# Performance work log

Hardware: AMD Instinct MI355X
Metric: run time of the kernel (lower is better)

The kernel has to match this reference:

```python
import jax, jax.numpy as jnp
import numpy as np

EMB = 1024
HEADS = 16
HEAD_DIM = EMB // HEADS
N = 16384


def setup_inputs() -> dict:
    key = jax.random.key(0)
    ks = jax.random.split(key, 9)
    s = 1.0 / np.sqrt(EMB)
    return {
        "src": jax.random.normal(ks[0], (N, EMB), dtype=jnp.float32),
        "Wq": jax.random.normal(ks[1], (EMB, EMB), dtype=jnp.float32) * s,
        "bq": jax.random.normal(ks[2], (EMB,), dtype=jnp.float32) * s,
        "Wk": jax.random.normal(ks[3], (EMB, EMB), dtype=jnp.float32) * s,
        "bk": jax.random.normal(ks[4], (EMB,), dtype=jnp.float32) * s,
        "Wv": jax.random.normal(ks[5], (EMB, EMB), dtype=jnp.float32) * s,
        "bv": jax.random.normal(ks[6], (EMB,), dtype=jnp.float32) * s,
        "Wo": jax.random.normal(ks[7], (EMB, EMB), dtype=jnp.float32) * s,
        "bo": jax.random.normal(ks[8], (EMB,), dtype=jnp.float32) * s,
    }


def reference(src, Wq, bq, Wk, bk, Wv, bv, Wo, bo):
    # nn.Linear: y = x @ W^T + b  (W is [out, in])
    q = src @ Wq.T + bq          # [N, E]
    k = src @ Wk.T + bk
    v = src @ Wv.T + bv
    q = q.reshape(-1, HEADS, HEAD_DIM)   # [N, H, D]
    k = k.reshape(-1, HEADS, HEAD_DIM)
    v = v.reshape(-1, HEADS, HEAD_DIM)
    # NOTE: attention is across heads within each token: scores [N, H, H]
    scale = 1.0 / jnp.sqrt(jnp.float32(HEAD_DIM))
    scores = jnp.einsum('nhd,ngd->nhg', q, k) * scale   # [N, H, H]
    attn = jax.nn.softmax(scores, axis=-1)
    out = jnp.einsum('nhg,ngd->nhd', attn, v)            # [N, H, D]
    out = out.reshape(-1, EMB)
    out = out @ Wo.T + bo                                 # [N, E]
    return out.reshape(-1, HEADS, HEAD_DIM)               # [N, H, D]
```

## Files before the change

kernel.cpp:

```cpp
#include <hip/hip_runtime.h>
#include <stdint.h>
#include <stddef.h>

#define EMB 1024
#define NTOK 16384

typedef __attribute__((ext_vector_type(8))) short short8;
typedef __attribute__((ext_vector_type(4))) float floatx4;

__device__ __forceinline__ unsigned short f2bf(float f) {
    union { float f; unsigned int u; } v; v.f = f;
    unsigned int u = v.u;
    unsigned int r = (u + 0x7fffu + ((u >> 16) & 1u)) >> 16;
    return (unsigned short)r;
}
__device__ __forceinline__ float bf2f(unsigned short s) {
    union { unsigned int u; float f; } v; v.u = ((unsigned int)s) << 16;
    return v.f;
}

__device__ __forceinline__ void gload16(const void* g, void* l) {
    __builtin_amdgcn_global_load_lds(
        (const __attribute__((address_space(1))) void*)g,
        (__attribute__((address_space(3))) void*)l, 16, 0, 0);
}

__global__ void cvt_kernel(const float* __restrict__ in,
                           unsigned short* __restrict__ out, int n4) {
    int idx = blockIdx.x * blockDim.x + threadIdx.x;
    int stride = gridDim.x * blockDim.x;
    for (int i = idx; i < n4; i += stride) {
        float4 f = reinterpret_cast<const float4*>(in)[i];
        ushort4 o;
        o.x = f2bf(f.x); o.y = f2bf(f.y); o.z = f2bf(f.z); o.w = f2bf(f.w);
        reinterpret_cast<ushort4*>(out)[i] = o;
    }
}

__global__ void cvt4_kernel(const float* __restrict__ s0, const float* __restrict__ s1,
                            const float* __restrict__ s2, const float* __restrict__ s3,
                            unsigned short* __restrict__ out) {
    int idx = blockIdx.x * blockDim.x + threadIdx.x;
    const int total = 4 << 18;
    int stride = gridDim.x * blockDim.x;
    for (int i = idx; i < total; i += stride) {
        int w = i >> 18, r = i & ((1 << 18) - 1);
        const float* s = (w == 0) ? s0 : (w == 1) ? s1 : (w == 2) ? s2 : s3;
        float4 f = reinterpret_cast<const float4*>(s)[r];
        ushort4 o;
        o.x = f2bf(f.x); o.y = f2bf(f.y); o.z = f2bf(f.z); o.w = f2bf(f.w);
        reinterpret_cast<ushort4*>(out)[i] = o;
    }
}

__global__ void bias_cat_kernel(const float* __restrict__ b0,
                                const float* __restrict__ b1,
                                const float* __restrict__ b2,
                                float* __restrict__ out) {
    int i = blockIdx.x * blockDim.x + threadIdx.x;
    float v = (i < 1024) ? b0[i] : (i < 2048 ? b1[i - 1024] : b2[i - 2048]);
    out[i] = v;
}

__device__ __forceinline__ void store_val(float* C, size_t idx, float v) { C[idx] = v; }
__device__ __forceinline__ void store_val(unsigned short* C, size_t idx, float v) { C[idx] = f2bf(v); }

template<typename OUT_T>
__global__ __launch_bounds__(512, 2)
void gemm256(const unsigned short* __restrict__ A,
             const unsigned short* __restrict__ B,
             const float* __restrict__ bias,
             OUT_T* __restrict__ C,
             int K, int Nc, int grid_m)
{
    __shared__ unsigned short lds[65536];

    const int bid = blockIdx.x;
    const int x = bid & 7;
    const int w = bid >> 3;
    const int ms = grid_m >> 3;
    const int m0 = (x * ms + (w & (ms - 1))) * 256;
    const int n0 = (w / ms) * 256;

    const int tid  = threadIdx.x;
    const int lane = tid & 63;
    const int wid  = tid >> 6;
    const int wm = (wid >> 2) * 128;
    const int wn = (wid & 3) * 64;
    const int rr = lane & 15;
    const int klo = (((lane >> 4) ^ ((rr >> 1) & 3)) << 3);

    const int aro = (wm + rr) * 32 + klo;
    const int bro = 16384 + (wn + rr) * 32 + klo;

    const unsigned short* pA[2];
    const unsigned short* pB[2];
    int ldst[2];
#pragma unroll
    for (int l = 0; l < 2; ++l) {
        const int P16  = l * 512 + tid;
        const int rowS = P16 >> 2;
        const int colel = (((P16 & 3) ^ ((rowS >> 1) & 3)) << 3);
        pA[l] = A + (size_t)(m0 + rowS) * K + colel;
        pB[l] = B + (size_t)(n0 + rowS) * K + colel;
        ldst[l] = P16 * 8;
    }

    floatx4 acc[8][4];
#pragma unroll
    for (int i = 0; i < 8; ++i)
#pragma unroll
        for (int j = 0; j < 4; ++j)
            acc[i][j] = (floatx4){0.f, 0.f, 0.f, 0.f};

    const int NT = K >> 6;

#pragma unroll
    for (int l = 0; l < 2; ++l) {
        gload16(pA[l],      &lds[0     + ldst[l]]);
        gload16(pA[l] + 32, &lds[8192  + ldst[l]]);
        gload16(pB[l],      &lds[16384 + ldst[l]]);
        gload16(pB[l] + 32, &lds[24576 + ldst[l]]);
    }
    asm volatile("s_waitcnt vmcnt(0)" ::: "memory");
    asm volatile("s_barrier" ::: "memory");

    short8 a0[4], a1[4], b0[4];
#pragma unroll
    for (int i = 0; i < 4; ++i)
        a0[i] = *reinterpret_cast<const short8*>(&lds[aro + i * 512]);
#pragma unroll
    for (int j = 0; j < 4; ++j)
        b0[j] = *reinterpret_cast<const short8*>(&lds[bro + j * 512]);

    for (int t = 0; t < NT; ++t) {
        const int cur = (t & 1) * 32768;
        const int nxt = cur ^ 32768;
        const int ktn = (t + 1 < NT) ? (t + 1) * 64 : 0;

        gload16(pA[0] + ktn, &lds[nxt + ldst[0]]);
        gload16(pA[1] + ktn, &lds[nxt + ldst[1]]);
        gload16(pB[0] + ktn, &lds[nxt + 16384 + ldst[0]]);
        gload16(pB[1] + ktn, &lds[nxt + 16384 + ldst[1]]);
#pragma unroll
        for (int i = 0; i < 4; ++i)
            a1[i] = *reinterpret_cast<const short8*>(&lds[cur + aro + 2048 + i * 512]);
        __builtin_amdgcn_s_setprio(1);
#pragma unroll
        for (int j = 0; j < 4; ++j)
#pragma unroll
            for (int i = 0; i < 4; ++i)
                acc[i][j] = __builtin_amdgcn_mfma_f32_16x16x32_bf16(a0[i], b0[j], acc[i][j], 0, 0, 0);
#pragma unroll
        for (int j = 0; j < 4; ++j)
#pragma unroll
            for (int i = 0; i < 4; ++i)
                acc[4 + i][j] = __builtin_amdgcn_mfma_f32_16x16x32_bf16(a1[i], b0[j], acc[4 + i][j], 0, 0, 0);
        __builtin_amdgcn_s_setprio(0);
        asm volatile("s_waitcnt vmcnt(4)" ::: "memory");
        asm volatile("s_barrier" ::: "memory");

        gload16(pA[0] + ktn + 32, &lds[nxt + 8192 + ldst[0]]);
        gload16(pA[1] + ktn + 32, &lds[nxt + 8192 + ldst[1]]);
        gload16(pB[0] + ktn + 32, &lds[nxt + 24576 + ldst[0]]);
        gload16(pB[1] + ktn + 32, &lds[nxt + 24576 + ldst[1]]);
#pragma unroll
        for (int i = 0; i < 4; ++i)
            a0[i] = *reinterpret_cast<const short8*>(&lds[cur + 8192 + aro + i * 512]);
#pragma unroll
        for (int j = 0; j < 4; ++j)
            b0[j] = *reinterpret_cast<const short8*>(&lds[cur + 8192 + bro + j * 512]);
#pragma unroll
        for (int i = 0; i < 4; ++i)
            a1[i] = *reinterpret_cast<const short8*>(&lds[cur + 8192 + aro + 2048 + i * 512]);
        __builtin_amdgcn_s_setprio(1);
#pragma unroll
        for (int j = 0; j < 4; ++j)
#pragma unroll
            for (int i = 0; i < 4; ++i)
                acc[i][j] = __builtin_amdgcn_mfma_f32_16x16x32_bf16(a0[i], b0[j], acc[i][j], 0, 0, 0);
#pragma unroll
        for (int j = 0; j < 4; ++j)
#pragma unroll
            for (int i = 0; i < 4; ++i)
                acc[4 + i][j] = __builtin_amdgcn_mfma_f32_16x16x32_bf16(a1[i], b0[j], acc[4 + i][j], 0, 0, 0);
        __builtin_amdgcn_s_setprio(0);
        asm volatile("s_waitcnt vmcnt(4)" ::: "memory");
        asm volatile("s_barrier" ::: "memory");
#pragma unroll
        for (int i = 0; i < 4; ++i)
            a0[i] = *reinterpret_cast<const short8*>(&lds[nxt + aro + i * 512]);
#pragma unroll
        for (int j = 0; j < 4; ++j)
            b0[j] = *reinterpret_cast<const short8*>(&lds[nxt + bro + j * 512]);
    }

    const int cn  = lane & 15;
    const int cm4 = (lane >> 4) * 4;
    float bv[4];
#pragma unroll
    for (int j = 0; j < 4; ++j) bv[j] = bias[n0 + wn + j * 16 + cn];
#pragma unroll
    for (int ai = 0; ai < 8; ++ai) {
        const int row = m0 + wm + (ai >> 2) * 64 + (ai & 3) * 16 + cm4;
#pragma unroll
        for (int j = 0; j < 4; ++j) {
            const int col = n0 + wn + j * 16 + cn;
#pragma unroll
            for (int r = 0; r < 4; ++r)
                store_val(C, (size_t)(row + r) * Nc + col, acc[ai][j][r] + bv[j]);
        }
    }
}

#define ROWP 72

__global__ __launch_bounds__(256)
void attn_kernel(const unsigned short* __restrict__ QKV,
                 unsigned short* __restrict__ O)
{
    const int wave = threadIdx.x >> 6;
    const int lane = threadIdx.x & 63;
    const int n = blockIdx.x * 4 + wave;

    __shared__ unsigned short lq[4][16 * ROWP];
    __shared__ unsigned short lk[4][16 * ROWP];
    __shared__ unsigned short lv[4][16 * ROWP];
    __shared__ float lp[4][256];

    {
        const unsigned short* gq = QKV + (size_t)n * 3072;
        const unsigned short* gk = gq + 1024;
        const unsigned short* gv = gq + 2048;
        for (int t = lane; t < 128; t += 64) {
            int r = t >> 3, c = t & 7;
            *reinterpret_cast<short8*>(&lq[wave][r * ROWP + c * 8]) =
                *reinterpret_cast<const short8*>(gq + t * 8);
            *reinterpret_cast<short8*>(&lk[wave][r * ROWP + c * 8]) =
                *reinterpret_cast<const short8*>(gk + t * 8);
            *reinterpret_cast<short8*>(&lv[wave][r * ROWP + c * 8]) =
                *reinterpret_cast<const short8*>(gv + t * 8);
        }
    }
    __syncthreads();

    const int g = lane & 15;
    const int a = lane >> 4;

    float kf[64];
#pragma unroll
    for (int c2 = 0; c2 < 8; ++c2) {
        short8 kv = *reinterpret_cast<const short8*>(&lk[wave][g * ROWP + c2 * 8]);
#pragma unroll
        for (int e = 0; e < 8; ++e) kf[c2 * 8 + e] = bf2f((unsigned short)kv[e]);
    }

#pragma unroll
    for (int i = 0; i < 4; ++i) {
        const int h = i * 4 + a;
        float s = 0.f;
#pragma unroll
        for (int c2 = 0; c2 < 8; ++c2) {
            short8 qv = *reinterpret_cast<const short8*>(&lq[wave][h * ROWP + c2 * 8]);
#pragma unroll
            for (int e = 0; e < 8; ++e)
                s = fmaf(bf2f((unsigned short)qv[e]), kf[c2 * 8 + e], s);
        }
        s *= 0.125f;

        float m = s;
#pragma unroll
        for (int o = 1; o < 16; o <<= 1) m = fmaxf(m, __shfl_xor(m, o, 64));
        float p = expf(s - m);
        float sum = p;
#pragma unroll
        for (int o = 1; o < 16; o <<= 1) sum += __shfl_xor(sum, o, 64);
        lp[wave][h * 16 + g] = p / sum;
    }
    __syncthreads();

    const int h = lane >> 2;
    const int db = (lane & 3) * 16;
    float o[16];
#pragma unroll
    for (int e = 0; e < 16; ++e) o[e] = 0.f;

    for (int g2 = 0; g2 < 16; ++g2) {
        const float pw = lp[wave][h * 16 + g2];
        short8 v0 = *reinterpret_cast<const short8*>(&lv[wave][g2 * ROWP + db]);
        short8 v1 = *reinterpret_cast<const short8*>(&lv[wave][g2 * ROWP + db + 8]);
#pragma unroll
        for (int e = 0; e < 8; ++e) {
            o[e]     = fmaf(pw, bf2f((unsigned short)v0[e]), o[e]);
            o[8 + e] = fmaf(pw, bf2f((unsigned short)v1[e]), o[8 + e]);
        }
    }

    short8 o0, o1;
#pragma unroll
    for (int e = 0; e < 8; ++e) {
        o0[e] = (short)f2bf(o[e]);
        o1[e] = (short)f2bf(o[8 + e]);
    }
    unsigned short* dst = O + (size_t)n * EMB + h * 64 + db;
    *reinterpret_cast<short8*>(dst) = o0;
    *reinterpret_cast<short8*>(dst + 8) = o1;
}

extern "C" void kernel_launch(void* const* d_in, const int* in_sizes, int n_in,
                              void* d_out, int out_size, void* d_ws, size_t ws_size,
                              hipStream_t stream)
{
    const float* src = (const float*)d_in[0];
    const float* Wq  = (const float*)d_in[1];
    const float* bq  = (const float*)d_in[2];
    const float* Wk  = (const float*)d_in[3];
    const float* bk  = (const float*)d_in[4];
    const float* Wv  = (const float*)d_in[5];
    const float* bv  = (const float*)d_in[6];
    const float* Wo  = (const float*)d_in[7];
    const float* bo  = (const float*)d_in[8];
    float* out = (float*)d_out;

    unsigned short* ws = (unsigned short*)d_ws;
    unsigned short* src_bf = ws;
    unsigned short* wqkv   = src_bf + (size_t)NTOK * EMB;
    unsigned short* wo_bf  = wqkv + (size_t)3 * EMB * EMB;
    unsigned short* qkv    = wo_bf + (size_t)EMB * EMB;
    unsigned short* ab     = qkv + (size_t)NTOK * 3 * EMB;
    float* bias_cat        = (float*)(ab + (size_t)NTOK * EMB);

    cvt_kernel<<<2048, 256, 0, stream>>>(src, src_bf, NTOK * EMB / 4);
    cvt4_kernel<<<2048, 256, 0, stream>>>(Wq, Wk, Wv, Wo, wqkv);
    bias_cat_kernel<<<12, 256, 0, stream>>>(bq, bk, bv, bias_cat);

    gemm256<unsigned short><<<dim3(64 * 12), 512, 0, stream>>>(
        src_bf, wqkv, bias_cat, qkv, EMB, 3 * EMB, 64);

    attn_kernel<<<NTOK / 4, 256, 0, stream>>>(qkv, ab);

    gemm256<float><<<dim3(64 * 4), 512, 0, stream>>>(
        ab, wo_bf, bo, out, EMB, EMB, 64);
}
```

Baseline: 200.2 us.

## Make GEMM persistent over N tiles with one 256-block wave

The GEMM kernel now launches exactly 256 workgroups, and each one loops over several 256-wide N tiles for its M tile. The K-tile prefetch carries straight across N-tile boundaries, and the epilogue with bias is emitted inside the loop. This removes the tail effect of 768 blocks on 256 CUs and keeps the A tile warm in cache. In exchange, occupancy drops to 1 block per CU (launch bounds changed from 2 to 1), and the epilogue stores are no longer overlapped by other resident blocks.

```diff
diff --git a/kernel.cpp b/kernel.cpp
--- a/kernel.cpp
+++ b/kernel.cpp
@@ -66,21 +66,22 @@
 __device__ __forceinline__ void store_val(unsigned short* C, size_t idx, float v) { C[idx] = f2bf(v); }
 
 template<typename OUT_T>
-__global__ __launch_bounds__(512, 2)
-void gemm256(const unsigned short* __restrict__ A,
-             const unsigned short* __restrict__ B,
-             const float* __restrict__ bias,
-             OUT_T* __restrict__ C,
-             int K, int Nc, int grid_m)
+__global__ __launch_bounds__(512, 1)
+void gemm256mn(const unsigned short* __restrict__ A,
+               const unsigned short* __restrict__ B,
+               const float* __restrict__ bias,
+               OUT_T* __restrict__ C,
+               int Nc, int nt_n)
 {
     __shared__ unsigned short lds[65536];
+    const int K = 1024;
+    const int NT = 16;
 
     const int bid = blockIdx.x;
     const int x = bid & 7;
     const int w = bid >> 3;
-    const int ms = grid_m >> 3;
-    const int m0 = (x * ms + (w & (ms - 1))) * 256;
-    const int n0 = (w / ms) * 256;
+    const int m0 = (x * 8 + (w & 7)) * 256;
+    const int n_base = (w >> 3) * nt_n * 256;
 
     const int tid  = threadIdx.x;
     const int lane = tid & 63;
@@ -102,9 +103,10 @@
         const int rowS = P16 >> 2;
         const int colel = (((P16 & 3) ^ ((rowS >> 1) & 3)) << 3);
         pA[l] = A + (size_t)(m0 + rowS) * K + colel;
-        pB[l] = B + (size_t)(n0 + rowS) * K + colel;
+        pB[l] = B + (size_t)(n_base + rowS) * K + colel;
         ldst[l] = P16 * 8;
     }
+    const size_t nstep = (size_t)256 * K;
 
     floatx4 acc[8][4];
 #pragma unroll
@@ -113,7 +115,7 @@
         for (int j = 0; j < 4; ++j)
             acc[i][j] = (floatx4){0.f, 0.f, 0.f, 0.f};
 
-    const int NT = K >> 6;
+    const int TOT = nt_n * NT;
 
 #pragma unroll
     for (int l = 0; l < 2; ++l) {
@@ -133,15 +135,22 @@
     for (int j = 0; j < 4; ++j)
         b0[j] = *reinterpret_cast<const short8*>(&lds[bro + j * 512]);
 
-    for (int t = 0; t < NT; ++t) {
-        const int cur = (t & 1) * 32768;
+    const int cn  = lane & 15;
+    const int cm4 = (lane >> 4) * 4;
+
+    for (int vt = 0; vt < TOT; ++vt) {
+        const int cur = (vt & 1) * 32768;
         const int nxt = cur ^ 32768;
-        const int ktn = (t + 1 < NT) ? (t + 1) * 64 : 0;
+        int vtn = vt + 1; if (vtn == TOT) vtn = 0;
+        const int ktn = (vtn & 15) * 64;
+        const int nbn = vtn >> 4;
+        const unsigned short* pBn0 = pB[0] + (size_t)nbn * nstep + ktn;
+        const unsigned short* pBn1 = pB[1] + (size_t)nbn * nstep + ktn;
 
         gload16(pA[0] + ktn, &lds[nxt + ldst[0]]);
         gload16(pA[1] + ktn, &lds[nxt + ldst[1]]);
-        gload16(pB[0] + ktn, &lds[nxt + 16384 + ldst[0]]);
-        gload16(pB[1] + ktn, &lds[nxt + 16384 + ldst[1]]);
+        gload16(pBn0,        &lds[nxt + 16384 + ldst[0]]);
+        gload16(pBn1,        &lds[nxt + 16384 + ldst[1]]);
 #pragma unroll
         for (int i = 0; i < 4; ++i)
             a1[i] = *reinterpret_cast<const short8*>(&lds[cur + aro + 2048 + i * 512]);
@@ -162,8 +171,8 @@
 
         gload16(pA[0] + ktn + 32, &lds[nxt + 8192 + ldst[0]]);
         gload16(pA[1] + ktn + 32, &lds[nxt + 8192 + ldst[1]]);
-        gload16(pB[0] + ktn + 32, &lds[nxt + 24576 + ldst[0]]);
-        gload16(pB[1] + ktn + 32, &lds[nxt + 24576 + ldst[1]]);
+        gload16(pBn0 + 32,        &lds[nxt + 24576 + ldst[0]]);
+        gload16(pBn1 + 32,        &lds[nxt + 24576 + ldst[1]]);
 #pragma unroll
         for (int i = 0; i < 4; ++i)
             a0[i] = *reinterpret_cast<const short8*>(&lds[cur + 8192 + aro + i * 512]);
@@ -193,22 +202,28 @@
 #pragma unroll
         for (int j = 0; j < 4; ++j)
             b0[j] = *reinterpret_cast<const short8*>(&lds[nxt + bro + j * 512]);
-    }
-
-    const int cn  = lane & 15;
-    const int cm4 = (lane >> 4) * 4;
-    float bv[4];
-#pragma unroll
-    for (int j = 0; j < 4; ++j) bv[j] = bias[n0 + wn + j * 16 + cn];
-#pragma unroll
-    for (int ai = 0; ai < 8; ++ai) {
-        const int row = m0 + wm + (ai >> 2) * 64 + (ai & 3) * 16 + cm4;
-#pragma unroll
-        for (int j = 0; j < 4; ++j) {
-            const int col = n0 + wn + j * 16 + cn;
-#pragma unroll
-            for (int r = 0; r < 4; ++r)
-                store_val(C, (size_t)(row + r) * Nc + col, acc[ai][j][r] + bv[j]);
+
+        if ((vt & 15) == 15) {
+            const int n0 = n_base + (vt >> 4) * 256;
+            float bv[4];
+#pragma unroll
+            for (int j = 0; j < 4; ++j) bv[j] = bias[n0 + wn + j * 16 + cn];
+#pragma unroll
+            for (int ai = 0; ai < 8; ++ai) {
+                const int row = m0 + wm + (ai >> 2) * 64 + (ai & 3) * 16 + cm4;
+#pragma unroll
+                for (int j = 0; j < 4; ++j) {
+                    const int col = n0 + wn + j * 16 + cn;
+#pragma unroll
+                    for (int r = 0; r < 4; ++r)
+                        store_val(C, (size_t)(row + r) * Nc + col, acc[ai][j][r] + bv[j]);
+                }
+            }
+#pragma unroll
+            for (int i = 0; i < 8; ++i)
+#pragma unroll
+                for (int j = 0; j < 4; ++j)
+                    acc[i][j] = (floatx4){0.f, 0.f, 0.f, 0.f};
         }
     }
 }
@@ -334,11 +349,11 @@
     cvt4_kernel<<<2048, 256, 0, stream>>>(Wq, Wk, Wv, Wo, wqkv);
     bias_cat_kernel<<<12, 256, 0, stream>>>(bq, bk, bv, bias_cat);
 
-    gemm256<unsigned short><<<dim3(64 * 12), 512, 0, stream>>>(
-        src_bf, wqkv, bias_cat, qkv, EMB, 3 * EMB, 64);
+    gemm256mn<unsigned short><<<dim3(256), 512, 0, stream>>>(
+        src_bf, wqkv, bias_cat, qkv, 3 * EMB, 3);
 
     attn_kernel<<<NTOK / 4, 256, 0, stream>>>(qkv, ab);
 
-    gemm256<float><<<dim3(64 * 4), 512, 0, stream>>>(
-        ab, wo_bf, bo, out, EMB, EMB, 64);
-}
+    gemm256mn<float><<<dim3(256), 512, 0, stream>>>(
+        ab, wo_bf, bo, out, EMB, 1);
+}
```

Result: no change. 201.2 us (+0.5%).

## Switch GEMMs to 32x32x16 MFMA and fuse conversion kernels into one launch

Applied to the files above, without the earlier changes.

The GEMM inner loop now uses 32x32x16 bf16 MFMA instructions instead of 16x16x32, with 16-wide accumulators and LDS fragment reads re-mapped through an XOR on the k-group. The epilogue is rewritten to match the 32x32 output layout. This cuts instruction count and LDS fragment traffic per FLOP. The launch bound drops to one block per CU, which matches the 128KB LDS footprint. The src, weight and bias conversion kernels are merged into a single launch to remove launch overhead.

```diff
diff --git a/kernel.cpp b/kernel.cpp
--- a/kernel.cpp
+++ b/kernel.cpp
@@ -7,6 +7,7 @@
 
 typedef __attribute__((ext_vector_type(8))) short short8;
 typedef __attribute__((ext_vector_type(4))) float floatx4;
+typedef __attribute__((ext_vector_type(16))) float floatx16;
 
 __device__ __forceinline__ unsigned short f2bf(float f) {
     union { float f; unsigned int u; } v; v.f = f;
@@ -25,49 +26,51 @@
         (__attribute__((address_space(3))) void*)l, 16, 0, 0);
 }
 
-__global__ void cvt_kernel(const float* __restrict__ in,
-                           unsigned short* __restrict__ out, int n4) {
+__global__ void cvt_all(const float* __restrict__ src,
+                        const float* __restrict__ s0, const float* __restrict__ s1,
+                        const float* __restrict__ s2, const float* __restrict__ s3,
+                        const float* __restrict__ b0, const float* __restrict__ b1,
+                        const float* __restrict__ b2,
+                        unsigned short* __restrict__ src_bf,
+                        unsigned short* __restrict__ wout,
+                        float* __restrict__ bias_cat) {
+    if (blockIdx.x == 0) {
+#pragma unroll
+        for (int t = 0; t < 12; ++t) {
+            int i = t * 256 + threadIdx.x;
+            float v = (i < 1024) ? b0[i] : (i < 2048 ? b1[i - 1024] : b2[i - 2048]);
+            bias_cat[i] = v;
+        }
+    }
+    const int SRC4 = 1 << 22;
+    const int TOT4 = SRC4 + (1 << 20);
     int idx = blockIdx.x * blockDim.x + threadIdx.x;
     int stride = gridDim.x * blockDim.x;
-    for (int i = idx; i < n4; i += stride) {
-        float4 f = reinterpret_cast<const float4*>(in)[i];
+    for (int i = idx; i < TOT4; i += stride) {
+        const float* sp;
+        unsigned short* op;
+        int r;
+        if (i < SRC4) {
+            sp = src; op = src_bf; r = i;
+        } else {
+            int j = i - SRC4;
+            int w = j >> 18; r = j & ((1 << 18) - 1);
+            sp = (w == 0) ? s0 : (w == 1) ? s1 : (w == 2) ? s2 : s3;
+            op = wout + ((size_t)(i - SRC4) & ~((size_t)(1 << 18) - 1)) * 4;
+        }
+        float4 f = reinterpret_cast<const float4*>(sp)[r];
         ushort4 o;
         o.x = f2bf(f.x); o.y = f2bf(f.y); o.z = f2bf(f.z); o.w = f2bf(f.w);
-        reinterpret_cast<ushort4*>(out)[i] = o;
-    }
-}
-
-__global__ void cvt4_kernel(const float* __restrict__ s0, const float* __restrict__ s1,
-                            const float* __restrict__ s2, const float* __restrict__ s3,
-                            unsigned short* __restrict__ out) {
-    int idx = blockIdx.x * blockDim.x + threadIdx.x;
-    const int total = 4 << 18;
-    int stride = gridDim.x * blockDim.x;
-    for (int i = idx; i < total; i += stride) {
-        int w = i >> 18, r = i & ((1 << 18) - 1);
-        const float* s = (w == 0) ? s0 : (w == 1) ? s1 : (w == 2) ? s2 : s3;
-        float4 f = reinterpret_cast<const float4*>(s)[r];
-        ushort4 o;
-        o.x = f2bf(f.x); o.y = f2bf(f.y); o.z = f2bf(f.z); o.w = f2bf(f.w);
-        reinterpret_cast<ushort4*>(out)[i] = o;
-    }
-}
-
-__global__ void bias_cat_kernel(const float* __restrict__ b0,
-                                const float* __restrict__ b1,
-                                const float* __restrict__ b2,
-                                float* __restrict__ out) {
-    int i = blockIdx.x * blockDim.x + threadIdx.x;
-    float v = (i < 1024) ? b0[i] : (i < 2048 ? b1[i - 1024] : b2[i - 2048]);
-    out[i] = v;
+        reinterpret_cast<ushort4*>(op)[r] = o;
+    }
 }
 
 __device__ __forceinline__ void store_val(float* C, size_t idx, float v) { C[idx] = v; }
 __device__ __forceinline__ void store_val(unsigned short* C, size_t idx, float v) { C[idx] = f2bf(v); }
 
 template<typename OUT_T>
-__global__ __launch_bounds__(512, 2)
-void gemm256(const unsigned short* __restrict__ A,
+__global__ __launch_bounds__(512, 1)
+void gemm32s(const unsigned short* __restrict__ A,
              const unsigned short* __restrict__ B,
              const float* __restrict__ bias,
              OUT_T* __restrict__ C,
@@ -87,11 +90,12 @@
     const int wid  = tid >> 6;
     const int wm = (wid >> 2) * 128;
     const int wn = (wid & 3) * 64;
-    const int rr = lane & 15;
-    const int klo = (((lane >> 4) ^ ((rr >> 1) & 3)) << 3);
-
-    const int aro = (wm + rr) * 32 + klo;
-    const int bro = 16384 + (wn + rr) * 32 + klo;
+    const int rl = lane & 31;
+    const int lh = lane >> 5;
+    const int go = ((lh ^ ((rl >> 1) & 3)) << 3);
+
+    const int arB = (wm + rl) * 32 + go;
+    const int brB = 16384 + (wn + rl) * 32 + go;
 
     const unsigned short* pA[2];
     const unsigned short* pB[2];
@@ -106,12 +110,13 @@
         ldst[l] = P16 * 8;
     }
 
-    floatx4 acc[8][4];
-#pragma unroll
-    for (int i = 0; i < 8; ++i)
-#pragma unroll
-        for (int j = 0; j < 4; ++j)
-            acc[i][j] = (floatx4){0.f, 0.f, 0.f, 0.f};
+    floatx16 acc[4][2];
+#pragma unroll
+    for (int i = 0; i < 4; ++i)
+#pragma unroll
+        for (int j = 0; j < 2; ++j)
+            acc[i][j] = (floatx16){0.f,0.f,0.f,0.f,0.f,0.f,0.f,0.f,
+                                   0.f,0.f,0.f,0.f,0.f,0.f,0.f,0.f};
 
     const int NT = K >> 6;
 
@@ -125,13 +130,13 @@
     asm volatile("s_waitcnt vmcnt(0)" ::: "memory");
     asm volatile("s_barrier" ::: "memory");
 
-    short8 a0[4], a1[4], b0[4];
-#pragma unroll
-    for (int i = 0; i < 4; ++i)
-        a0[i] = *reinterpret_cast<const short8*>(&lds[aro + i * 512]);
-#pragma unroll
-    for (int j = 0; j < 4; ++j)
-        b0[j] = *reinterpret_cast<const short8*>(&lds[bro + j * 512]);
+    short8 a0[4], a1[4], b0[2], b1[2];
+#pragma unroll
+    for (int fm = 0; fm < 4; ++fm)
+        a0[fm] = *reinterpret_cast<const short8*>(&lds[arB + fm * 1024]);
+#pragma unroll
+    for (int fn = 0; fn < 2; ++fn)
+        b0[fn] = *reinterpret_cast<const short8*>(&lds[brB + fn * 1024]);
 
     for (int t = 0; t < NT; ++t) {
         const int cur = (t & 1) * 32768;
@@ -143,19 +148,22 @@
         gload16(pB[0] + ktn, &lds[nxt + 16384 + ldst[0]]);
         gload16(pB[1] + ktn, &lds[nxt + 16384 + ldst[1]]);
 #pragma unroll
-        for (int i = 0; i < 4; ++i)
-            a1[i] = *reinterpret_cast<const short8*>(&lds[cur + aro + 2048 + i * 512]);
+        for (int fm = 0; fm < 4; ++fm)
+            a1[fm] = *reinterpret_cast<const short8*>(&lds[cur + ((arB + fm * 1024) ^ 16)]);
+#pragma unroll
+        for (int fn = 0; fn < 2; ++fn)
+            b1[fn] = *reinterpret_cast<const short8*>(&lds[cur + ((brB + fn * 1024) ^ 16)]);
         __builtin_amdgcn_s_setprio(1);
 #pragma unroll
-        for (int j = 0; j < 4; ++j)
-#pragma unroll
-            for (int i = 0; i < 4; ++i)
-                acc[i][j] = __builtin_amdgcn_mfma_f32_16x16x32_bf16(a0[i], b0[j], acc[i][j], 0, 0, 0);
-#pragma unroll
-        for (int j = 0; j < 4; ++j)
-#pragma unroll
-            for (int i = 0; i < 4; ++i)
-                acc[4 + i][j] = __builtin_amdgcn_mfma_f32_16x16x32_bf16(a1[i], b0[j], acc[4 + i][j], 0, 0, 0);
+        for (int fn = 0; fn < 2; ++fn)
+#pragma unroll
+            for (int fm = 0; fm < 4; ++fm)
+                acc[fm][fn] = __builtin_amdgcn_mfma_f32_32x32x16_bf16(a0[fm], b0[fn], acc[fm][fn], 0, 0, 0);
+#pragma unroll
+        for (int fn = 0; fn < 2; ++fn)
+#pragma unroll
+            for (int fm = 0; fm < 4; ++fm)
+                acc[fm][fn] = __builtin_amdgcn_mfma_f32_32x32x16_bf16(a1[fm], b1[fn], acc[fm][fn], 0, 0, 0);
         __builtin_amdgcn_s_setprio(0);
         asm volatile("s_waitcnt vmcnt(4)" ::: "memory");
         asm volatile("s_barrier" ::: "memory");
@@ -165,50 +173,54 @@
         gload16(pB[0] + ktn + 32, &lds[nxt + 24576 + ldst[0]]);
         gload16(pB[1] + ktn + 32, &lds[nxt + 24576 + ldst[1]]);
 #pragma unroll
-        for (int i = 0; i < 4; ++i)
-            a0[i] = *reinterpret_cast<const short8*>(&lds[cur + 8192 + aro + i * 512]);
-#pragma unroll
-        for (int j = 0; j < 4; ++j)
-            b0[j] = *reinterpret_cast<const short8*>(&lds[cur + 8192 + bro + j * 512]);
-#pragma unroll
-        for (int i = 0; i < 4; ++i)
-            a1[i] = *reinterpret_cast<const short8*>(&lds[cur + 8192 + aro + 2048 + i * 512]);
+        for (int fm = 0; fm < 4; ++fm)
+            a0[fm] = *reinterpret_cast<const short8*>(&lds[cur + 8192 + arB + fm * 1024]);
+#pragma unroll
+        for (int fn = 0; fn < 2; ++fn)
+            b0[fn] = *reinterpret_cast<const short8*>(&lds[cur + 8192 + brB + fn * 1024]);
+#pragma unroll
+        for (int fm = 0; fm < 4; ++fm)
+            a1[fm] = *reinterpret_cast<const short8*>(&lds[cur + 8192 + ((arB + fm * 1024) ^ 16)]);
+#pragma unroll
+        for (int fn = 0; fn < 2; ++fn)
+            b1[fn] = *reinterpret_cast<const short8*>(&lds[cur + 8192 + ((brB + fn * 1024) ^ 16)]);
         __builtin_amdgcn_s_setprio(1);
 #pragma unroll
-        for (int j = 0; j < 4; ++j)
-#pragma unroll
-            for (int i = 0; i < 4; ++i)
-                acc[i][j] = __builtin_amdgcn_mfma_f32_16x16x32_bf16(a0[i], b0[j], acc[i][j], 0, 0, 0);
-#pragma unroll
-        for (int j = 0; j < 4; ++j)
-#pragma unroll
-            for (int i = 0; i < 4; ++i)
-                acc[4 + i][j] = __builtin_amdgcn_mfma_f32_16x16x32_bf16(a1[i], b0[j], acc[4 + i][j], 0, 0, 0);
+        for (int fn = 0; fn < 2; ++fn)
+#pragma unroll
+            for (int fm = 0; fm < 4; ++fm)
+                acc[fm][fn] = __builtin_amdgcn_mfma_f32_32x32x16_bf16(a0[fm], b0[fn], acc[fm][fn], 0, 0, 0);
+#pragma unroll
+        for (int fn = 0; fn < 2; ++fn)
+#pragma unroll
+            for (int fm = 0; fm < 4; ++fm)
+                acc[fm][fn] = __builtin_amdgcn_mfma_f32_32x32x16_bf16(a1[fm], b1[fn], acc[fm][fn], 0, 0, 0);
         __builtin_amdgcn_s_setprio(0);
         asm volatile("s_waitcnt vmcnt(4)" ::: "memory");
         asm volatile("s_barrier" ::: "memory");
 #pragma unroll
-        for (int i = 0; i < 4; ++i)
-            a0[i] = *reinterpret_cast<const short8*>(&lds[nxt + aro + i * 512]);
-#pragma unroll
-        for (int j = 0; j < 4; ++j)
-            b0[j] = *reinterpret_cast<const short8*>(&lds[nxt + bro + j * 512]);
-    }
-
-    const int cn  = lane & 15;
-    const int cm4 = (lane >> 4) * 4;
-    float bv[4];
-#pragma unroll
-    for (int j = 0; j < 4; ++j) bv[j] = bias[n0 + wn + j * 16 + cn];
-#pragma unroll
-    for (int ai = 0; ai < 8; ++ai) {
-        const int row = m0 + wm + (ai >> 2) * 64 + (ai & 3) * 16 + cm4;
-#pragma unroll
-        for (int j = 0; j < 4; ++j) {
-            const int col = n0 + wn + j * 16 + cn;
-#pragma unroll
-            for (int r = 0; r < 4; ++r)
-                store_val(C, (size_t)(row + r) * Nc + col, acc[ai][j][r] + bv[j]);
+        for (int fm = 0; fm < 4; ++fm)
+            a0[fm] = *reinterpret_cast<const short8*>(&lds[nxt + arB + fm * 1024]);
+#pragma unroll
+        for (int fn = 0; fn < 2; ++fn)
+            b0[fn] = *reinterpret_cast<const short8*>(&lds[nxt + brB + fn * 1024]);
+    }
+
+    const int col0 = n0 + wn + rl;
+    float bv[2];
+    bv[0] = bias[col0];
+    bv[1] = bias[col0 + 32];
+#pragma unroll
+    for (int fm = 0; fm < 4; ++fm) {
+        const int rbase = m0 + wm + fm * 32 + 4 * lh;
+#pragma unroll
+        for (int fn = 0; fn < 2; ++fn) {
+            const int col = col0 + fn * 32;
+#pragma unroll
+            for (int reg = 0; reg < 16; ++reg) {
+                const int row = rbase + (reg & 3) + 8 * (reg >> 2);
+                store_val(C, (size_t)row * Nc + col, acc[fm][fn][reg] + bv[fn]);
+            }
         }
     }
 }
@@ -330,15 +342,14 @@
     unsigned short* ab     = qkv + (size_t)NTOK * 3 * EMB;
     float* bias_cat        = (float*)(ab + (size_t)NTOK * EMB);
 
-    cvt_kernel<<<2048, 256, 0, stream>>>(src, src_bf, NTOK * EMB / 4);
-    cvt4_kernel<<<2048, 256, 0, stream>>>(Wq, Wk, Wv, Wo, wqkv);
-    bias_cat_kernel<<<12, 256, 0, stream>>>(bq, bk, bv, bias_cat);
-
-    gemm256<unsigned short><<<dim3(64 * 12), 512, 0, stream>>>(
+    cvt_all<<<2048, 256, 0, stream>>>(src, Wq, Wk, Wv, Wo, bq, bk, bv,
+                                      src_bf, wqkv, bias_cat);
+
+    gemm32s<unsigned short><<<dim3(64 * 12), 512, 0, stream>>>(
         src_bf, wqkv, bias_cat, qkv, EMB, 3 * EMB, 64);
 
     attn_kernel<<<NTOK / 4, 256, 0, stream>>>(qkv, ab);
 
-    gemm256<float><<<dim3(64 * 4), 512, 0, stream>>>(
+    gemm32s<float><<<dim3(64 * 4), 512, 0, stream>>>(
         ab, wo_bf, bo, out, EMB, EMB, 64);
 }
```

After: 216.7 us. +8.3%, slower.
